# Kernel optimization log

Hardware: AMD Instinct MI355X
Metric: run time of the kernel (lower is better)

The kernel has to match this reference:

```python
import jax, jax.numpy as jnp
import numpy as np
from jax import lax

B, T, I, H = 256, 512, 128, 256


def setup_inputs() -> dict:
    key = jax.random.key(0)
    ks = jax.random.split(key, 11)
    s = 1.0 / np.sqrt(H)  # PyTorch LSTM/Linear default init range
    u = lambda k, shape: jax.random.uniform(k, shape, jnp.float32, -s, s)
    return {
        "x": jax.random.uniform(ks[0], (B, T, I), jnp.float32),
        "enc_W_ih": u(ks[1], (4 * H, I)),
        "enc_W_hh": u(ks[2], (4 * H, H)),
        "enc_b_ih": u(ks[3], (4 * H,)),
        "enc_b_hh": u(ks[4], (4 * H,)),
        "dec_W_ih": u(ks[5], (4 * H, I)),
        "dec_W_hh": u(ks[6], (4 * H, H)),
        "dec_b_ih": u(ks[7], (4 * H,)),
        "dec_b_hh": u(ks[8], (4 * H,)),
        "lin_W": u(ks[9], (I, H)),
        "lin_b": u(ks[10], (I,)),
    }


def _lstm_cell(xt, h, c, W_ih, W_hh, b):
    # PyTorch gate order: input, forget, cell(g), output
    gates = xt @ W_ih.T + h @ W_hh.T + b  # [B, 4H]
    i, f, g, o = jnp.split(gates, 4, axis=-1)
    c_new = jax.nn.sigmoid(f) * c + jax.nn.sigmoid(i) * jnp.tanh(g)
    h_new = jax.nn.sigmoid(o) * jnp.tanh(c_new)
    return h_new, c_new


def reference(x, enc_W_ih, enc_W_hh, enc_b_ih, enc_b_hh,
              dec_W_ih, dec_W_hh, dec_b_ih, dec_b_hh, lin_W, lin_b):
    batch, max_len, _ = x.shape
    b_enc = enc_b_ih + enc_b_hh
    b_dec = dec_b_ih + dec_b_hh

    # ---- encoder: standard forward LSTM, keep only final (h, c) ----
    def enc_step(carry, xt):
        h, c = carry
        h, c = _lstm_cell(xt, h, c, enc_W_ih, enc_W_hh, b_enc)
        return (h, c), None

    h0 = jnp.zeros((batch, H), x.dtype)
    c0 = jnp.zeros((batch, H), x.dtype)
    (h, c), _ = lax.scan(enc_step, (h0, c0), x.transpose(1, 0, 2))  # xs: [T,B,I]

    # prediction at the last timestep comes from encoder final hidden state
    pred_last = jax.nn.sigmoid(h @ lin_W.T + lin_b)  # [B, I]

    # ---- decoder: run backwards in time, feeding previous prediction ----
    # (inference path of the module: decoder_input = predicted_outputs[:, t+1].data,
    #  i.e. fed-back prediction is DETACHED -> stop_gradient)
    def dec_step(carry, _):
        h, c, pred = carry
        inp = lax.stop_gradient(pred)
        h, c = _lstm_cell(inp, h, c, dec_W_ih, dec_W_hh, b_dec)
        pred = jax.nn.sigmoid(h @ lin_W.T + lin_b)
        return (h, c, pred), pred

    _, preds = lax.scan(dec_step, (h, c, pred_last), None, length=max_len - 1)
    # preds[k] is the prediction at time t = max_len-2-k; flip into forward order
    out = jnp.concatenate([preds[::-1], pred_last[None]], axis=0)  # [T, B, I]
    return out.transpose(1, 0, 2)  # [B, T, I]
```

## Files before the change

### kernel.cpp

```cpp
#include <hip/hip_runtime.h>


typedef __bf16 bf16;
typedef bf16 bf16x8 __attribute__((ext_vector_type(8)));
typedef float f32x4 __attribute__((ext_vector_type(4)));
typedef unsigned u32;
typedef u32 u32x4 __attribute__((ext_vector_type(4)));

#define MFMA16(a, b, c) __builtin_amdgcn_mfma_f32_16x16x32_bf16((a), (b), (c), 0, 0, 0)
#define AT_STORE_DEV(p, v) __hip_atomic_store((p), (v), __ATOMIC_RELAXED, __HIP_MEMORY_SCOPE_AGENT)

__device__ __forceinline__ float sigm(float x) { return 1.0f / (1.0f + __expf(-x)); }
__device__ __forceinline__ float tanhfast(float x) { return 1.0f - 2.0f / (__expf(2.0f * x) + 1.0f); }

__device__ __forceinline__ u32x4 load_hx4(const u32* p) {
    u32x4 v;
    asm volatile("global_load_dwordx4 %0, %1, off sc0 sc1" : "=v"(v) : "v"(p));
    return v;
}
__device__ __forceinline__ void store_h(u32* p, u32 v) {
    asm volatile("global_store_dword %0, %1, off sc0 sc1" :: "v"(p), "v"(v) : "memory");
}
__device__ __forceinline__ u32 load_flag(const u32* p) {
    u32 v;
    asm volatile("global_load_dword %0, %1, off sc0 sc1\n\ts_waitcnt vmcnt(0)"
                 : "=v"(v) : "v"(p) : "memory");
    return v;
}

__global__ void pack_kernel(const float* __restrict__ eWih, const float* __restrict__ eWhh,
                            const float* __restrict__ dWih, const float* __restrict__ dWhh,
                            const float* __restrict__ linW,
                            bf16* __restrict__ encB, bf16* __restrict__ decB, bf16* __restrict__ linB) {
    int idx = blockIdx.x * 256 + threadIdx.x;
    if (idx < 786432) {
        int which = idx / 393216;
        int id = idx % 393216;
        int cg = id / 24576;
        int rem = id % 24576;
        int ks = rem / 2048;
        int n = (rem / 512) & 3;
        int lane = (rem >> 3) & 63;
        int e = rem & 7;
        int k = ks * 32 + (lane >> 4) * 8 + e;
        int col = n * 256 + cg * 16 + (lane & 15);
        const float* Wih = which ? dWih : eWih;
        const float* Whh = which ? dWhh : eWhh;
        float v = (k < 128) ? Wih[col * 128 + k] : Whh[col * 256 + (k - 128)];
        (which ? decB : encB)[id] = (bf16)v;
    } else if (idx < 819200) {
        int i3 = idx - 786432;
        int ks = i3 >> 12;
        int n = (i3 >> 9) & 7;
        int lane = (i3 >> 3) & 63;
        int e = i3 & 7;
        int k = ks * 32 + (lane >> 4) * 8 + e;
        int col = n * 16 + (lane & 15);
        linB[i3] = (bf16)linW[col * 256 + k];
    }
}

__global__ void zero_kernel(unsigned* __restrict__ p) {
    int i = blockIdx.x * 256 + threadIdx.x;
    if (i < 65792) AT_STORE_DEV(&p[i], 0u);
}

__global__ __launch_bounds__(256, 1)
void lstm_main(const float* __restrict__ x,
               const float* __restrict__ eb_ih, const float* __restrict__ eb_hh,
               const float* __restrict__ db_ih, const float* __restrict__ db_hh,
               const float* __restrict__ lin_b,
               const bf16* __restrict__ encB, const bf16* __restrict__ decB,
               const bf16* __restrict__ linB,
               u32* __restrict__ hbuf32, u32* __restrict__ flags,
               float* __restrict__ out) {
    __shared__ bf16 Bg[24576];
    __shared__ bf16 Lw[32768];
    __shared__ bf16 Pst[4 * 16 * 136];

    const int bid = blockIdx.x;
    const int rg = bid >> 4;
    const int cg = bid & 15;
    const int tid = threadIdx.x;
    const int w = tid >> 6;
    const int lane = tid & 63;
    const int l15 = lane & 15, l4 = lane >> 4;
    const int rbase = rg * 64 + w * 16;
    const int ucol = cg * 16 + l15;
    const int arow = rbase + l15;
    const int k0 = l4 * 8;
    const int prow = rbase + l4 * 4;

    const int rt = rg * 4 + w;
    const int htile_w = (cg >> 1) * 256;
    const int hgrp = ((cg & 1) * 2 + (l15 >> 3)) * 16;
    const int widx = (l15 & 7) >> 1;

    {
        const f32x4* src = (const f32x4*)(encB + cg * 24576);
        f32x4* dst = (f32x4*)Bg;
        #pragma unroll
        for (int i = 0; i < 12; i++) dst[tid + 256 * i] = src[tid + 256 * i];
    }
    float bias_g[4];
    #pragma unroll
    for (int g = 0; g < 4; g++) bias_g[g] = eb_ih[g * 256 + ucol] + eb_hh[g * 256 + ucol];
    __syncthreads();

    u32* myflag = flags + rg * 64 + cg;
    const u32* pollp = flags + rg * 64 + l15;
    u32 stepno = 0;
    float c[4] = {0.f, 0.f, 0.f, 0.f};

    const float* xrow = x + (size_t)arow * 512 * 128 + k0;

    f32x4 xr[8];
    #pragma unroll
    for (int i = 0; i < 4; i++) {
        xr[2 * i]     = *(const f32x4*)(xrow + i * 32);
        xr[2 * i + 1] = *(const f32x4*)(xrow + i * 32 + 4);
    }

    for (int t = 0; t < 512; t++) {
        const u32* hr32 = hbuf32 + (t & 1) * 32768;
        u32* hw32 = hbuf32 + ((t + 1) & 1) * 32768;

        u32x4 hv[8];
        const u32* hb = hr32 + rt * 2048 + lane * 4;
        #pragma unroll
        for (int ks = 0; ks < 8; ks++) hv[ks] = load_hx4(hb + ks * 256);

        f32x4 acc[4];
        #pragma unroll
        for (int n = 0; n < 4; n++) acc[n] = (f32x4){0.f, 0.f, 0.f, 0.f};

        #pragma unroll
        for (int ks = 0; ks < 4; ks++) {
            f32x4 xa = xr[2 * ks], xb = xr[2 * ks + 1];
            bf16x8 a;
            a[0] = (bf16)xa[0]; a[1] = (bf16)xa[1]; a[2] = (bf16)xa[2]; a[3] = (bf16)xa[3];
            a[4] = (bf16)xb[0]; a[5] = (bf16)xb[1]; a[6] = (bf16)xb[2]; a[7] = (bf16)xb[3];
            #pragma unroll
            for (int n = 0; n < 4; n++) {
                bf16x8 b = *(const bf16x8*)&Bg[((ks * 4 + n) * 64 + lane) * 8];
                acc[n] = MFMA16(a, b, acc[n]);
            }
        }
        asm volatile("s_waitcnt vmcnt(0)" ::: "memory");
        __builtin_amdgcn_sched_barrier(0);
        #pragma unroll
        for (int ks = 0; ks < 8; ks++) {
            bf16x8 a = __builtin_bit_cast(bf16x8, hv[ks]);
            #pragma unroll
            for (int n = 0; n < 4; n++) {
                bf16x8 b = *(const bf16x8*)&Bg[(((ks + 4) * 4 + n) * 64 + lane) * 8];
                acc[n] = MFMA16(a, b, acc[n]);
            }
        }
        #pragma unroll
        for (int r = 0; r < 4; r++) {
            float gi = sigm(acc[0][r] + bias_g[0]);
            float gf = sigm(acc[1][r] + bias_g[1]);
            float gg = tanhfast(acc[2][r] + bias_g[2]);
            float go = sigm(acc[3][r] + bias_g[3]);
            c[r] = gf * c[r] + gi * gg;
            float h = go * tanhfast(c[r]);
            unsigned hvv = (unsigned)__builtin_bit_cast(unsigned short, (bf16)h);
            unsigned hp = __shfl_xor(hvv, 1);
            if (!(lane & 1))
                store_h(&hw32[rt * 2048 + htile_w + (hgrp + l4 * 4 + r) * 4 + widx],
                        hvv | (hp << 16));
        }
        stepno++;
        __syncthreads();
        if (tid == 0) store_h(myflag, stepno);
        int tn = t < 511 ? t + 1 : 511;
        #pragma unroll
        for (int i = 0; i < 4; i++) {
            xr[2 * i]     = *(const f32x4*)(xrow + (size_t)tn * 128 + i * 32);
            xr[2 * i + 1] = *(const f32x4*)(xrow + (size_t)tn * 128 + i * 32 + 4);
        }
        while (!__all((int)(load_flag(pollp) >= stepno))) __builtin_amdgcn_s_sleep(1);
    }

    {
        const f32x4* src = (const f32x4*)(decB + cg * 24576);
        f32x4* dst = (f32x4*)Bg;
        #pragma unroll
        for (int i = 0; i < 12; i++) dst[tid + 256 * i] = src[tid + 256 * i];
        const f32x4* s2 = (const f32x4*)linB;
        f32x4* d2 = (f32x4*)Lw;
        #pragma unroll
        for (int i = 0; i < 16; i++) d2[tid + 256 * i] = s2[tid + 256 * i];
    }
    #pragma unroll
    for (int g = 0; g < 4; g++) bias_g[g] = db_ih[g * 256 + ucol] + db_hh[g * 256 + ucol];
    float lbias[8];
    #pragma unroll
    for (int n = 0; n < 8; n++) lbias[n] = lin_b[n * 16 + l15];
    __syncthreads();

    const int ncg = cg >> 1;
    const int hsel = cg & 1;

    for (int k = 0; k < 512; k++) {
        const u32* hr32 = hbuf32 + (k & 1) * 32768;

        u32x4 hv[8];
        const u32* hb = hr32 + rt * 2048 + lane * 4;
        #pragma unroll
        for (int ks = 0; ks < 8; ks++) hv[ks] = load_hx4(hb + ks * 256);
        asm volatile("s_waitcnt vmcnt(0)" ::: "memory");
        __builtin_amdgcn_sched_barrier(0);
        bf16x8 ha[8];
        #pragma unroll
        for (int ks = 0; ks < 8; ks++) ha[ks] = __builtin_bit_cast(bf16x8, hv[ks]);

        f32x4 pacc[8];
        #pragma unroll
        for (int n = 0; n < 8; n++) pacc[n] = (f32x4){0.f, 0.f, 0.f, 0.f};
        #pragma unroll
        for (int ks = 0; ks < 8; ks++) {
            #pragma unroll
            for (int n = 0; n < 8; n++) {
                bf16x8 b = *(const bf16x8*)&Lw[((ks * 8 + n) * 64 + lane) * 8];
                pacc[n] = MFMA16(ha[ks], b, pacc[n]);
            }
        }
        const int t_out = 511 - k;
        float* obase = out + (size_t)prow * 512 * 128 + (size_t)t_out * 128;
        bf16* pst_w = Pst + w * 2176;
        #pragma unroll
        for (int n = 0; n < 8; n++) {
            #pragma unroll
            for (int r = 0; r < 4; r++) {
                float p = sigm(pacc[n][r] + lbias[n]);
                pst_w[(l4 * 4 + r) * 136 + n * 16 + l15] = (bf16)p;
                if (n == ncg && (l15 >> 3) == hsel)
                    obase[(size_t)r * 512 * 128 + n * 16 + l15] = p;
            }
        }
        if (k == 511) break;

        f32x4 acc[4];
        #pragma unroll
        for (int n = 0; n < 4; n++) acc[n] = (f32x4){0.f, 0.f, 0.f, 0.f};
        #pragma unroll
        for (int ks = 0; ks < 8; ks++) {
            #pragma unroll
            for (int n = 0; n < 4; n++) {
                bf16x8 b = *(const bf16x8*)&Bg[(((ks + 4) * 4 + n) * 64 + lane) * 8];
                acc[n] = MFMA16(ha[ks], b, acc[n]);
            }
        }
        const bf16* pst_r = Pst + w * 2176 + l15 * 136 + k0;
        #pragma unroll
        for (int ks = 0; ks < 4; ks++) {
            bf16x8 a = *(const bf16x8*)(pst_r + ks * 32);
            #pragma unroll
            for (int n = 0; n < 4; n++) {
                bf16x8 b = *(const bf16x8*)&Bg[((ks * 4 + n) * 64 + lane) * 8];
                acc[n] = MFMA16(a, b, acc[n]);
            }
        }
        u32* hw32 = hbuf32 + ((k + 1) & 1) * 32768;
        #pragma unroll
        for (int r = 0; r < 4; r++) {
            float gi = sigm(acc[0][r] + bias_g[0]);
            float gf = sigm(acc[1][r] + bias_g[1]);
            float gg = tanhfast(acc[2][r] + bias_g[2]);
            float go = sigm(acc[3][r] + bias_g[3]);
            c[r] = gf * c[r] + gi * gg;
            float h = go * tanhfast(c[r]);
            unsigned hvv = (unsigned)__builtin_bit_cast(unsigned short, (bf16)h);
            unsigned hp = __shfl_xor(hvv, 1);
            if (!(lane & 1))
                store_h(&hw32[rt * 2048 + htile_w + (hgrp + l4 * 4 + r) * 4 + widx],
                        hvv | (hp << 16));
        }
        stepno++;
        __syncthreads();
        if (tid == 0) store_h(myflag, stepno);
        while (!__all((int)(load_flag(pollp) >= stepno))) __builtin_amdgcn_s_sleep(1);
    }
}

extern "C" void kernel_launch(void* const* d_in, const int* in_sizes, int n_in,
                              void* d_out, int out_size, void* d_ws, size_t ws_size,
                              hipStream_t stream) {
    const float* x    = (const float*)d_in[0];
    const float* eWih = (const float*)d_in[1];
    const float* eWhh = (const float*)d_in[2];
    const float* ebih = (const float*)d_in[3];
    const float* ebhh = (const float*)d_in[4];
    const float* dWih = (const float*)d_in[5];
    const float* dWhh = (const float*)d_in[6];
    const float* dbih = (const float*)d_in[7];
    const float* dbhh = (const float*)d_in[8];
    const float* linW = (const float*)d_in[9];
    const float* linb = (const float*)d_in[10];
    float* out = (float*)d_out;

    bf16* encB = (bf16*)d_ws;
    bf16* decB = encB + 393216;
    bf16* linB = decB + 393216;
    u32*  hbuf = (u32*)(linB + 32768);
    u32*  flags = hbuf + 65536;

    hipLaunchKernelGGL(pack_kernel, dim3(3200), dim3(256), 0, stream,
                       eWih, eWhh, dWih, dWhh, linW, encB, decB, linB);
    hipLaunchKernelGGL(zero_kernel, dim3(257), dim3(256), 0, stream, hbuf);
    hipLaunchKernelGGL(lstm_main, dim3(64), dim3(256), 0, stream,
                       x, ebih, ebhh, dbih, dbhh, linb, encB, decB, linB, hbuf, flags, out);
}
```

Before: 4.866 ms.

## Use per-wave flags instead of block barriers in recurrent LSTM steps

Replaces the per-block __syncthreads plus a single block flag with per-wavefront flags indexed by row tile, so each wave publishes its h slice and waits only on the 16 column-group waves that share its rows. The flag wait moves to the start of each step, the next x prefetch is issued earlier, and output stores are deferred until after the flag is published, keeping them off the critical path. The spin loop gains a bounded iteration cap, which could let a wave proceed before its data is ready if a peer is slow.

```diff
diff --git a/kernel.cpp b/kernel.cpp
--- a/kernel.cpp
+++ b/kernel.cpp
@@ -27,6 +27,26 @@
                  : "=v"(v) : "v"(p) : "memory");
     return v;
 }
+__device__ __forceinline__ f32x4 load_x4a(const float* p) {
+    f32x4 v;
+    asm volatile("global_load_dwordx4 %0, %1, off" : "=v"(v) : "v"(p));
+    return v;
+}
+__device__ __forceinline__ void store_f32a(float* p, float v) {
+    asm volatile("global_store_dword %0, %1, off" :: "v"(p), "v"(v) : "memory");
+}
+#define DRAIN0() do { asm volatile("s_waitcnt vmcnt(0)" ::: "memory"); \
+                      __builtin_amdgcn_sched_barrier(0); } while (0)
+
+#define FLAG_GATE(rtag)                                                          \
+    {                                                                            \
+        int spins = 0;                                                           \
+        while (!__all((int)(load_flag(pollp) >= (u32)(rtag)))) {                 \
+            if (++spins > (1 << 17)) break;                                      \
+            __builtin_amdgcn_s_sleep(1);                                         \
+        }                                                                        \
+        __builtin_amdgcn_sched_barrier(0);                                       \
+    }
 
 __global__ void pack_kernel(const float* __restrict__ eWih, const float* __restrict__ eWhh,
                             const float* __restrict__ dWih, const float* __restrict__ dWhh,
@@ -96,6 +116,9 @@
     const int hgrp = ((cg & 1) * 2 + (l15 >> 3)) * 16;
     const int widx = (l15 & 7) >> 1;
 
+    u32* myflag = flags + rt * 16 + cg;
+    const u32* pollp = flags + rt * 16 + l15;
+
     {
         const f32x4* src = (const f32x4*)(encB + cg * 24576);
         f32x4* dst = (f32x4*)Bg;
@@ -107,23 +130,21 @@
     for (int g = 0; g < 4; g++) bias_g[g] = eb_ih[g * 256 + ucol] + eb_hh[g * 256 + ucol];
     __syncthreads();
 
-    u32* myflag = flags + rg * 64 + cg;
-    const u32* pollp = flags + rg * 64 + l15;
-    u32 stepno = 0;
     float c[4] = {0.f, 0.f, 0.f, 0.f};
-
     const float* xrow = x + (size_t)arow * 512 * 128 + k0;
 
     f32x4 xr[8];
     #pragma unroll
     for (int i = 0; i < 4; i++) {
-        xr[2 * i]     = *(const f32x4*)(xrow + i * 32);
-        xr[2 * i + 1] = *(const f32x4*)(xrow + i * 32 + 4);
+        xr[2 * i]     = load_x4a(xrow + i * 32);
+        xr[2 * i + 1] = load_x4a(xrow + i * 32 + 4);
     }
 
     for (int t = 0; t < 512; t++) {
         const u32* hr32 = hbuf32 + (t & 1) * 32768;
         u32* hw32 = hbuf32 + ((t + 1) & 1) * 32768;
+
+        FLAG_GATE(t);
 
         u32x4 hv[8];
         const u32* hb = hr32 + rt * 2048 + lane * 4;
@@ -146,8 +167,15 @@
                 acc[n] = MFMA16(a, b, acc[n]);
             }
         }
-        asm volatile("s_waitcnt vmcnt(0)" ::: "memory");
-        __builtin_amdgcn_sched_barrier(0);
+        DRAIN0();
+
+        int tn = t < 511 ? t + 1 : 511;
+        #pragma unroll
+        for (int i = 0; i < 4; i++) {
+            xr[2 * i]     = load_x4a(xrow + (size_t)tn * 128 + i * 32);
+            xr[2 * i + 1] = load_x4a(xrow + (size_t)tn * 128 + i * 32 + 4);
+        }
+
         #pragma unroll
         for (int ks = 0; ks < 8; ks++) {
             bf16x8 a = __builtin_bit_cast(bf16x8, hv[ks]);
@@ -171,18 +199,11 @@
                 store_h(&hw32[rt * 2048 + htile_w + (hgrp + l4 * 4 + r) * 4 + widx],
                         hvv | (hp << 16));
         }
-        stepno++;
-        __syncthreads();
-        if (tid == 0) store_h(myflag, stepno);
-        int tn = t < 511 ? t + 1 : 511;
-        #pragma unroll
-        for (int i = 0; i < 4; i++) {
-            xr[2 * i]     = *(const f32x4*)(xrow + (size_t)tn * 128 + i * 32);
-            xr[2 * i + 1] = *(const f32x4*)(xrow + (size_t)tn * 128 + i * 32 + 4);
-        }
-        while (!__all((int)(load_flag(pollp) >= stepno))) __builtin_amdgcn_s_sleep(1);
-    }
-
+        DRAIN0();
+        if (lane == 0) store_h(myflag, (u32)(t + 1));
+    }
+
+    __syncthreads();
     {
         const f32x4* src = (const f32x4*)(decB + cg * 24576);
         f32x4* dst = (f32x4*)Bg;
@@ -193,8 +214,9 @@
         #pragma unroll
         for (int i = 0; i < 16; i++) d2[tid + 256 * i] = s2[tid + 256 * i];
     }
+    float bias_d[4];
     #pragma unroll
-    for (int g = 0; g < 4; g++) bias_g[g] = db_ih[g * 256 + ucol] + db_hh[g * 256 + ucol];
+    for (int g = 0; g < 4; g++) bias_d[g] = db_ih[g * 256 + ucol] + db_hh[g * 256 + ucol];
     float lbias[8];
     #pragma unroll
     for (int n = 0; n < 8; n++) lbias[n] = lin_b[n * 16 + l15];
@@ -205,13 +227,15 @@
 
     for (int k = 0; k < 512; k++) {
         const u32* hr32 = hbuf32 + (k & 1) * 32768;
+        const u32 rtag = (u32)(512 + k);
+
+        FLAG_GATE(rtag);
 
         u32x4 hv[8];
         const u32* hb = hr32 + rt * 2048 + lane * 4;
         #pragma unroll
         for (int ks = 0; ks < 8; ks++) hv[ks] = load_hx4(hb + ks * 256);
-        asm volatile("s_waitcnt vmcnt(0)" ::: "memory");
-        __builtin_amdgcn_sched_barrier(0);
+        DRAIN0();
         bf16x8 ha[8];
         #pragma unroll
         for (int ks = 0; ks < 8; ks++) ha[ks] = __builtin_bit_cast(bf16x8, hv[ks]);
@@ -236,11 +260,17 @@
             for (int r = 0; r < 4; r++) {
                 float p = sigm(pacc[n][r] + lbias[n]);
                 pst_w[(l4 * 4 + r) * 136 + n * 16 + l15] = (bf16)p;
-                if (n == ncg && (l15 >> 3) == hsel)
-                    obase[(size_t)r * 512 * 128 + n * 16 + l15] = p;
-            }
-        }
-        if (k == 511) break;
+            }
+        }
+        if (k == 511) {
+            #pragma unroll
+            for (int r = 0; r < 4; r++) {
+                float p = sigm(pacc[ncg][r] + lbias[ncg]);
+                if ((l15 >> 3) == hsel)
+                    store_f32a(&obase[(size_t)r * 512 * 128 + ncg * 16 + l15], p);
+            }
+            break;
+        }
 
         f32x4 acc[4];
         #pragma unroll
@@ -266,10 +296,10 @@
         u32* hw32 = hbuf32 + ((k + 1) & 1) * 32768;
         #pragma unroll
         for (int r = 0; r < 4; r++) {
-            float gi = sigm(acc[0][r] + bias_g[0]);
-            float gf = sigm(acc[1][r] + bias_g[1]);
-            float gg = tanhfast(acc[2][r] + bias_g[2]);
-            float go = sigm(acc[3][r] + bias_g[3]);
+            float gi = sigm(acc[0][r] + bias_d[0]);
+            float gf = sigm(acc[1][r] + bias_d[1]);
+            float gg = tanhfast(acc[2][r] + bias_d[2]);
+            float go = sigm(acc[3][r] + bias_d[3]);
             c[r] = gf * c[r] + gi * gg;
             float h = go * tanhfast(c[r]);
             unsigned hvv = (unsigned)__builtin_bit_cast(unsigned short, (bf16)h);
@@ -278,10 +308,14 @@
                 store_h(&hw32[rt * 2048 + htile_w + (hgrp + l4 * 4 + r) * 4 + widx],
                         hvv | (hp << 16));
         }
-        stepno++;
-        __syncthreads();
-        if (tid == 0) store_h(myflag, stepno);
-        while (!__all((int)(load_flag(pollp) >= stepno))) __builtin_amdgcn_s_sleep(1);
+        DRAIN0();
+        if (lane == 0) store_h(myflag, (u32)(rtag + 1));
+        #pragma unroll
+        for (int r = 0; r < 4; r++) {
+            float p = sigm(pacc[ncg][r] + lbias[ncg]);
+            if ((l15 >> 3) == hsel)
+                store_f32a(&obase[(size_t)r * 512 * 128 + ncg * 16 + l15], p);
+        }
     }
 }
 
```

Result: slower. 5.645 ms (+16.0%).

## Map row groups to XCCs and use XCC-local coherence for h exchange

Applied to the files above, without the earlier changes.

Launches 256 blocks. Each block reads its hardware XCC id and claims a slot with an atomic counter, so each row group (rg) is placed on one XCC and its 16 column groups exchange h and step flags only among blocks sharing that XCC's L2. A canary handshake checks that local visibility works; if it does, the loads and stores drop the sc1 (device-scope) bits, otherwise the code falls back to device-scope coherence. Surplus blocks exit right away. Spin loops gain timeout breaks. The gain depends on blocks being scheduled evenly across XCCs, and the timeouts could silently break correctness.

```diff
diff --git a/kernel.cpp b/kernel.cpp
--- a/kernel.cpp
+++ b/kernel.cpp
@@ -13,17 +13,41 @@
 __device__ __forceinline__ float sigm(float x) { return 1.0f / (1.0f + __expf(-x)); }
 __device__ __forceinline__ float tanhfast(float x) { return 1.0f - 2.0f / (__expf(2.0f * x) + 1.0f); }
 
-__device__ __forceinline__ u32x4 load_hx4(const u32* p) {
+template<bool LOC> __device__ __forceinline__ u32x4 ld_h4(const u32* p) {
     u32x4 v;
-    asm volatile("global_load_dwordx4 %0, %1, off sc0 sc1" : "=v"(v) : "v"(p));
+    if constexpr (LOC) asm volatile("global_load_dwordx4 %0, %1, off sc0" : "=v"(v) : "v"(p));
+    else               asm volatile("global_load_dwordx4 %0, %1, off sc0 sc1" : "=v"(v) : "v"(p));
     return v;
 }
-__device__ __forceinline__ void store_h(u32* p, u32 v) {
+template<bool LOC> __device__ __forceinline__ void st_h(u32* p, u32 v) {
+    if constexpr (LOC) asm volatile("global_store_dword %0, %1, off" :: "v"(p), "v"(v) : "memory");
+    else               asm volatile("global_store_dword %0, %1, off sc0 sc1" :: "v"(p), "v"(v) : "memory");
+}
+template<bool LOC> __device__ __forceinline__ u32 ld_flag(const u32* p) {
+    u32 v;
+    if constexpr (LOC)
+        asm volatile("global_load_dword %0, %1, off sc0\n\ts_waitcnt vmcnt(0)"
+                     : "=v"(v) : "v"(p) : "memory");
+    else
+        asm volatile("global_load_dword %0, %1, off sc0 sc1\n\ts_waitcnt vmcnt(0)"
+                     : "=v"(v) : "v"(p) : "memory");
+    return v;
+}
+__device__ __forceinline__ void st_dev(u32* p, u32 v) {
     asm volatile("global_store_dword %0, %1, off sc0 sc1" :: "v"(p), "v"(v) : "memory");
 }
-__device__ __forceinline__ u32 load_flag(const u32* p) {
+__device__ __forceinline__ u32 ld_dev(const u32* p) {
     u32 v;
     asm volatile("global_load_dword %0, %1, off sc0 sc1\n\ts_waitcnt vmcnt(0)"
+                 : "=v"(v) : "v"(p) : "memory");
+    return v;
+}
+__device__ __forceinline__ void st_plain(u32* p, u32 v) {
+    asm volatile("global_store_dword %0, %1, off" :: "v"(p), "v"(v) : "memory");
+}
+__device__ __forceinline__ u32 ld_sc0(const u32* p) {
+    u32 v;
+    asm volatile("global_load_dword %0, %1, off sc0\n\ts_waitcnt vmcnt(0)"
                  : "=v"(v) : "v"(p) : "memory");
     return v;
 }
@@ -62,7 +86,234 @@
 
 __global__ void zero_kernel(unsigned* __restrict__ p) {
     int i = blockIdx.x * 256 + threadIdx.x;
-    if (i < 65792) AT_STORE_DEV(&p[i], 0u);
+    if (i < 66312) AT_STORE_DEV(&p[i], 0u);
+}
+
+template<bool LOC>
+__device__ void run_chains(int rg, int cg, int tid,
+                           const float* __restrict__ x,
+                           const float* __restrict__ eb_ih, const float* __restrict__ eb_hh,
+                           const float* __restrict__ db_ih, const float* __restrict__ db_hh,
+                           const float* __restrict__ lin_b,
+                           const bf16* __restrict__ encB, const bf16* __restrict__ decB,
+                           const bf16* __restrict__ linB,
+                           u32* __restrict__ hbuf32, u32* __restrict__ flags,
+                           float* __restrict__ out,
+                           bf16* Bg, bf16* Lw, bf16* Pst) {
+    const int w = tid >> 6;
+    const int lane = tid & 63;
+    const int l15 = lane & 15, l4 = lane >> 4;
+    const int rbase = rg * 64 + w * 16;
+    const int ucol = cg * 16 + l15;
+    const int arow = rbase + l15;
+    const int k0 = l4 * 8;
+    const int prow = rbase + l4 * 4;
+
+    const int rt = rg * 4 + w;
+    const int htile_w = (cg >> 1) * 256;
+    const int hgrp = ((cg & 1) * 2 + (l15 >> 3)) * 16;
+    const int widx = (l15 & 7) >> 1;
+
+    {
+        const f32x4* src = (const f32x4*)(encB + cg * 24576);
+        f32x4* dst = (f32x4*)Bg;
+        #pragma unroll
+        for (int i = 0; i < 12; i++) dst[tid + 256 * i] = src[tid + 256 * i];
+    }
+    float bias_g[4];
+    #pragma unroll
+    for (int g = 0; g < 4; g++) bias_g[g] = eb_ih[g * 256 + ucol] + eb_hh[g * 256 + ucol];
+    __syncthreads();
+
+    u32* myflag = flags + rg * 64 + cg;
+    const u32* pollp = flags + rg * 64 + l15;
+    u32 stepno = 0;
+    float c[4] = {0.f, 0.f, 0.f, 0.f};
+
+    const float* xrow = x + (size_t)arow * 512 * 128 + k0;
+
+    f32x4 xr[8];
+    #pragma unroll
+    for (int i = 0; i < 4; i++) {
+        xr[2 * i]     = *(const f32x4*)(xrow + i * 32);
+        xr[2 * i + 1] = *(const f32x4*)(xrow + i * 32 + 4);
+    }
+
+    for (int t = 0; t < 512; t++) {
+        const u32* hr32 = hbuf32 + (t & 1) * 32768;
+        u32* hw32 = hbuf32 + ((t + 1) & 1) * 32768;
+
+        u32x4 hv[8];
+        const u32* hb = hr32 + rt * 2048 + lane * 4;
+        #pragma unroll
+        for (int ks = 0; ks < 8; ks++) hv[ks] = ld_h4<LOC>(hb + ks * 256);
+
+        f32x4 acc[4];
+        #pragma unroll
+        for (int n = 0; n < 4; n++) acc[n] = (f32x4){0.f, 0.f, 0.f, 0.f};
+
+        #pragma unroll
+        for (int ks = 0; ks < 4; ks++) {
+            f32x4 xa = xr[2 * ks], xb = xr[2 * ks + 1];
+            bf16x8 a;
+            a[0] = (bf16)xa[0]; a[1] = (bf16)xa[1]; a[2] = (bf16)xa[2]; a[3] = (bf16)xa[3];
+            a[4] = (bf16)xb[0]; a[5] = (bf16)xb[1]; a[6] = (bf16)xb[2]; a[7] = (bf16)xb[3];
+            #pragma unroll
+            for (int n = 0; n < 4; n++) {
+                bf16x8 b = *(const bf16x8*)&Bg[((ks * 4 + n) * 64 + lane) * 8];
+                acc[n] = MFMA16(a, b, acc[n]);
+            }
+        }
+        asm volatile("s_waitcnt vmcnt(0)" ::: "memory");
+        __builtin_amdgcn_sched_barrier(0);
+        #pragma unroll
+        for (int ks = 0; ks < 8; ks++) {
+            bf16x8 a = __builtin_bit_cast(bf16x8, hv[ks]);
+            #pragma unroll
+            for (int n = 0; n < 4; n++) {
+                bf16x8 b = *(const bf16x8*)&Bg[(((ks + 4) * 4 + n) * 64 + lane) * 8];
+                acc[n] = MFMA16(a, b, acc[n]);
+            }
+        }
+        #pragma unroll
+        for (int r = 0; r < 4; r++) {
+            float gi = sigm(acc[0][r] + bias_g[0]);
+            float gf = sigm(acc[1][r] + bias_g[1]);
+            float gg = tanhfast(acc[2][r] + bias_g[2]);
+            float go = sigm(acc[3][r] + bias_g[3]);
+            c[r] = gf * c[r] + gi * gg;
+            float h = go * tanhfast(c[r]);
+            unsigned hvv = (unsigned)__builtin_bit_cast(unsigned short, (bf16)h);
+            unsigned hp = __shfl_xor(hvv, 1);
+            if (!(lane & 1))
+                st_h<LOC>(&hw32[rt * 2048 + htile_w + (hgrp + l4 * 4 + r) * 4 + widx],
+                          hvv | (hp << 16));
+        }
+        stepno++;
+        __syncthreads();
+        if (tid == 0) st_h<LOC>(myflag, stepno);
+        int tn = t < 511 ? t + 1 : 511;
+        #pragma unroll
+        for (int i = 0; i < 4; i++) {
+            xr[2 * i]     = *(const f32x4*)(xrow + (size_t)tn * 128 + i * 32);
+            xr[2 * i + 1] = *(const f32x4*)(xrow + (size_t)tn * 128 + i * 32 + 4);
+        }
+        {
+            int sp = 0;
+            while (!__all((int)(ld_flag<LOC>(pollp) >= stepno))) {
+                if (++sp > 8192) break;
+                __builtin_amdgcn_s_sleep(1);
+            }
+        }
+    }
+
+    {
+        const f32x4* src = (const f32x4*)(decB + cg * 24576);
+        f32x4* dst = (f32x4*)Bg;
+        #pragma unroll
+        for (int i = 0; i < 12; i++) dst[tid + 256 * i] = src[tid + 256 * i];
+        const f32x4* s2 = (const f32x4*)linB;
+        f32x4* d2 = (f32x4*)Lw;
+        #pragma unroll
+        for (int i = 0; i < 16; i++) d2[tid + 256 * i] = s2[tid + 256 * i];
+    }
+    float bias_d[4];
+    #pragma unroll
+    for (int g = 0; g < 4; g++) bias_d[g] = db_ih[g * 256 + ucol] + db_hh[g * 256 + ucol];
+    float lbias[8];
+    #pragma unroll
+    for (int n = 0; n < 8; n++) lbias[n] = lin_b[n * 16 + l15];
+    __syncthreads();
+
+    const int ncg = cg >> 1;
+    const int hsel = cg & 1;
+
+    for (int k = 0; k < 512; k++) {
+        const u32* hr32 = hbuf32 + (k & 1) * 32768;
+
+        u32x4 hv[8];
+        const u32* hb = hr32 + rt * 2048 + lane * 4;
+        #pragma unroll
+        for (int ks = 0; ks < 8; ks++) hv[ks] = ld_h4<LOC>(hb + ks * 256);
+        asm volatile("s_waitcnt vmcnt(0)" ::: "memory");
+        __builtin_amdgcn_sched_barrier(0);
+        bf16x8 ha[8];
+        #pragma unroll
+        for (int ks = 0; ks < 8; ks++) ha[ks] = __builtin_bit_cast(bf16x8, hv[ks]);
+
+        f32x4 pacc[8];
+        #pragma unroll
+        for (int n = 0; n < 8; n++) pacc[n] = (f32x4){0.f, 0.f, 0.f, 0.f};
+        #pragma unroll
+        for (int ks = 0; ks < 8; ks++) {
+            #pragma unroll
+            for (int n = 0; n < 8; n++) {
+                bf16x8 b = *(const bf16x8*)&Lw[((ks * 8 + n) * 64 + lane) * 8];
+                pacc[n] = MFMA16(ha[ks], b, pacc[n]);
+            }
+        }
+        const int t_out = 511 - k;
+        float* obase = out + (size_t)prow * 512 * 128 + (size_t)t_out * 128;
+        bf16* pst_w = Pst + w * 2176;
+        #pragma unroll
+        for (int n = 0; n < 8; n++) {
+            #pragma unroll
+            for (int r = 0; r < 4; r++) {
+                float p = sigm(pacc[n][r] + lbias[n]);
+                pst_w[(l4 * 4 + r) * 136 + n * 16 + l15] = (bf16)p;
+                if (n == ncg && (l15 >> 3) == hsel)
+                    obase[(size_t)r * 512 * 128 + n * 16 + l15] = p;
+            }
+        }
+        if (k == 511) break;
+
+        f32x4 acc[4];
+        #pragma unroll
+        for (int n = 0; n < 4; n++) acc[n] = (f32x4){0.f, 0.f, 0.f, 0.f};
+        #pragma unroll
+        for (int ks = 0; ks < 8; ks++) {
+            #pragma unroll
+            for (int n = 0; n < 4; n++) {
+                bf16x8 b = *(const bf16x8*)&Bg[(((ks + 4) * 4 + n) * 64 + lane) * 8];
+                acc[n] = MFMA16(ha[ks], b, acc[n]);
+            }
+        }
+        const bf16* pst_r = Pst + w * 2176 + l15 * 136 + k0;
+        #pragma unroll
+        for (int ks = 0; ks < 4; ks++) {
+            bf16x8 a = *(const bf16x8*)(pst_r + ks * 32);
+            #pragma unroll
+            for (int n = 0; n < 4; n++) {
+                bf16x8 b = *(const bf16x8*)&Bg[((ks * 4 + n) * 64 + lane) * 8];
+                acc[n] = MFMA16(a, b, acc[n]);
+            }
+        }
+        u32* hw32 = hbuf32 + ((k + 1) & 1) * 32768;
+        #pragma unroll
+        for (int r = 0; r < 4; r++) {
+            float gi = sigm(acc[0][r] + bias_d[0]);
+            float gf = sigm(acc[1][r] + bias_d[1]);
+            float gg = tanhfast(acc[2][r] + bias_d[2]);
+            float go = sigm(acc[3][r] + bias_d[3]);
+            c[r] = gf * c[r] + gi * gg;
+            float h = go * tanhfast(c[r]);
+            unsigned hvv = (unsigned)__builtin_bit_cast(unsigned short, (bf16)h);
+            unsigned hp = __shfl_xor(hvv, 1);
+            if (!(lane & 1))
+                st_h<LOC>(&hw32[rt * 2048 + htile_w + (hgrp + l4 * 4 + r) * 4 + widx],
+                          hvv | (hp << 16));
+        }
+        stepno++;
+        __syncthreads();
+        if (tid == 0) st_h<LOC>(myflag, stepno);
+        {
+            int sp = 0;
+            while (!__all((int)(ld_flag<LOC>(pollp) >= stepno))) {
+                if (++sp > 8192) break;
+                __builtin_amdgcn_s_sleep(1);
+            }
+        }
+    }
 }
 
 __global__ __launch_bounds__(256, 1)
@@ -77,212 +328,58 @@
     __shared__ bf16 Bg[24576];
     __shared__ bf16 Lw[32768];
     __shared__ bf16 Pst[4 * 16 * 136];
-
-    const int bid = blockIdx.x;
-    const int rg = bid >> 4;
-    const int cg = bid & 15;
+    __shared__ int s_role[2];
+
     const int tid = threadIdx.x;
-    const int w = tid >> 6;
-    const int lane = tid & 63;
-    const int l15 = lane & 15, l4 = lane >> 4;
-    const int rbase = rg * 64 + w * 16;
-    const int ucol = cg * 16 + l15;
-    const int arow = rbase + l15;
-    const int k0 = l4 * 8;
-    const int prow = rbase + l4 * 4;
-
-    const int rt = rg * 4 + w;
-    const int htile_w = (cg >> 1) * 256;
-    const int hgrp = ((cg & 1) * 2 + (l15 >> 3)) * 16;
-    const int widx = (l15 & 7) >> 1;
-
+    u32* xslot  = flags + 256;
+    u32* boot   = flags + 264;
+    u32* canary = flags + 520;
+
+    if (tid == 0) {
+        u32 xcc;
+        asm("s_getreg_b32 %0, hwreg(HW_REG_XCC_ID)" : "=s"(xcc));
+        xcc &= 7;
+        u32 slot = __hip_atomic_fetch_add(&xslot[xcc], 1u,
+                                          __ATOMIC_RELAXED, __HIP_MEMORY_SCOPE_AGENT);
+        s_role[0] = (int)xcc;
+        s_role[1] = (int)slot;
+    }
+    __syncthreads();
+    const int rg = s_role[0];
+    const int cg = s_role[1];
+    if (rg >= 4 || cg >= 16) return;
+
+    if (tid == 0) {
+        st_plain(&canary[rg * 64 + cg], 1u);
+        const u32* pc = &canary[rg * 64 + ((cg + 1) & 15)];
+        u32 ok = 0;
+        for (int i = 0; i < 4096; i++) {
+            if (ld_sc0(pc) == 1u) { ok = 1; break; }
+            __builtin_amdgcn_s_sleep(1);
+        }
+        st_dev(&boot[rg * 64 + cg], ok ? 2u : 1u);
+    }
+    __syncthreads();
+
+    const int l15v = tid & 15;
+    u32 myv = 0;
     {
-        const f32x4* src = (const f32x4*)(encB + cg * 24576);
-        f32x4* dst = (f32x4*)Bg;
-        #pragma unroll
-        for (int i = 0; i < 12; i++) dst[tid + 256 * i] = src[tid + 256 * i];
-    }
-    float bias_g[4];
-    #pragma unroll
-    for (int g = 0; g < 4; g++) bias_g[g] = eb_ih[g * 256 + ucol] + eb_hh[g * 256 + ucol];
-    __syncthreads();
-
-    u32* myflag = flags + rg * 64 + cg;
-    const u32* pollp = flags + rg * 64 + l15;
-    u32 stepno = 0;
-    float c[4] = {0.f, 0.f, 0.f, 0.f};
-
-    const float* xrow = x + (size_t)arow * 512 * 128 + k0;
-
-    f32x4 xr[8];
-    #pragma unroll
-    for (int i = 0; i < 4; i++) {
-        xr[2 * i]     = *(const f32x4*)(xrow + i * 32);
-        xr[2 * i + 1] = *(const f32x4*)(xrow + i * 32 + 4);
-    }
-
-    for (int t = 0; t < 512; t++) {
-        const u32* hr32 = hbuf32 + (t & 1) * 32768;
-        u32* hw32 = hbuf32 + ((t + 1) & 1) * 32768;
-
-        u32x4 hv[8];
-        const u32* hb = hr32 + rt * 2048 + lane * 4;
-        #pragma unroll
-        for (int ks = 0; ks < 8; ks++) hv[ks] = load_hx4(hb + ks * 256);
-
-        f32x4 acc[4];
-        #pragma unroll
-        for (int n = 0; n < 4; n++) acc[n] = (f32x4){0.f, 0.f, 0.f, 0.f};
-
-        #pragma unroll
-        for (int ks = 0; ks < 4; ks++) {
-            f32x4 xa = xr[2 * ks], xb = xr[2 * ks + 1];
-            bf16x8 a;
-            a[0] = (bf16)xa[0]; a[1] = (bf16)xa[1]; a[2] = (bf16)xa[2]; a[3] = (bf16)xa[3];
-            a[4] = (bf16)xb[0]; a[5] = (bf16)xb[1]; a[6] = (bf16)xb[2]; a[7] = (bf16)xb[3];
-            #pragma unroll
-            for (int n = 0; n < 4; n++) {
-                bf16x8 b = *(const bf16x8*)&Bg[((ks * 4 + n) * 64 + lane) * 8];
-                acc[n] = MFMA16(a, b, acc[n]);
-            }
-        }
-        asm volatile("s_waitcnt vmcnt(0)" ::: "memory");
-        __builtin_amdgcn_sched_barrier(0);
-        #pragma unroll
-        for (int ks = 0; ks < 8; ks++) {
-            bf16x8 a = __builtin_bit_cast(bf16x8, hv[ks]);
-            #pragma unroll
-            for (int n = 0; n < 4; n++) {
-                bf16x8 b = *(const bf16x8*)&Bg[(((ks + 4) * 4 + n) * 64 + lane) * 8];
-                acc[n] = MFMA16(a, b, acc[n]);
-            }
-        }
-        #pragma unroll
-        for (int r = 0; r < 4; r++) {
-            float gi = sigm(acc[0][r] + bias_g[0]);
-            float gf = sigm(acc[1][r] + bias_g[1]);
-            float gg = tanhfast(acc[2][r] + bias_g[2]);
-            float go = sigm(acc[3][r] + bias_g[3]);
-            c[r] = gf * c[r] + gi * gg;
-            float h = go * tanhfast(c[r]);
-            unsigned hvv = (unsigned)__builtin_bit_cast(unsigned short, (bf16)h);
-            unsigned hp = __shfl_xor(hvv, 1);
-            if (!(lane & 1))
-                store_h(&hw32[rt * 2048 + htile_w + (hgrp + l4 * 4 + r) * 4 + widx],
-                        hvv | (hp << 16));
-        }
-        stepno++;
-        __syncthreads();
-        if (tid == 0) store_h(myflag, stepno);
-        int tn = t < 511 ? t + 1 : 511;
-        #pragma unroll
-        for (int i = 0; i < 4; i++) {
-            xr[2 * i]     = *(const f32x4*)(xrow + (size_t)tn * 128 + i * 32);
-            xr[2 * i + 1] = *(const f32x4*)(xrow + (size_t)tn * 128 + i * 32 + 4);
-        }
-        while (!__all((int)(load_flag(pollp) >= stepno))) __builtin_amdgcn_s_sleep(1);
-    }
-
-    {
-        const f32x4* src = (const f32x4*)(decB + cg * 24576);
-        f32x4* dst = (f32x4*)Bg;
-        #pragma unroll
-        for (int i = 0; i < 12; i++) dst[tid + 256 * i] = src[tid + 256 * i];
-        const f32x4* s2 = (const f32x4*)linB;
-        f32x4* d2 = (f32x4*)Lw;
-        #pragma unroll
-        for (int i = 0; i < 16; i++) d2[tid + 256 * i] = s2[tid + 256 * i];
-    }
-    #pragma unroll
-    for (int g = 0; g < 4; g++) bias_g[g] = db_ih[g * 256 + ucol] + db_hh[g * 256 + ucol];
-    float lbias[8];
-    #pragma unroll
-    for (int n = 0; n < 8; n++) lbias[n] = lin_b[n * 16 + l15];
-    __syncthreads();
-
-    const int ncg = cg >> 1;
-    const int hsel = cg & 1;
-
-    for (int k = 0; k < 512; k++) {
-        const u32* hr32 = hbuf32 + (k & 1) * 32768;
-
-        u32x4 hv[8];
-        const u32* hb = hr32 + rt * 2048 + lane * 4;
-        #pragma unroll
-        for (int ks = 0; ks < 8; ks++) hv[ks] = load_hx4(hb + ks * 256);
-        asm volatile("s_waitcnt vmcnt(0)" ::: "memory");
-        __builtin_amdgcn_sched_barrier(0);
-        bf16x8 ha[8];
-        #pragma unroll
-        for (int ks = 0; ks < 8; ks++) ha[ks] = __builtin_bit_cast(bf16x8, hv[ks]);
-
-        f32x4 pacc[8];
-        #pragma unroll
-        for (int n = 0; n < 8; n++) pacc[n] = (f32x4){0.f, 0.f, 0.f, 0.f};
-        #pragma unroll
-        for (int ks = 0; ks < 8; ks++) {
-            #pragma unroll
-            for (int n = 0; n < 8; n++) {
-                bf16x8 b = *(const bf16x8*)&Lw[((ks * 8 + n) * 64 + lane) * 8];
-                pacc[n] = MFMA16(ha[ks], b, pacc[n]);
-            }
-        }
-        const int t_out = 511 - k;
-        float* obase = out + (size_t)prow * 512 * 128 + (size_t)t_out * 128;
-        bf16* pst_w = Pst + w * 2176;
-        #pragma unroll
-        for (int n = 0; n < 8; n++) {
-            #pragma unroll
-            for (int r = 0; r < 4; r++) {
-                float p = sigm(pacc[n][r] + lbias[n]);
-                pst_w[(l4 * 4 + r) * 136 + n * 16 + l15] = (bf16)p;
-                if (n == ncg && (l15 >> 3) == hsel)
-                    obase[(size_t)r * 512 * 128 + n * 16 + l15] = p;
-            }
-        }
-        if (k == 511) break;
-
-        f32x4 acc[4];
-        #pragma unroll
-        for (int n = 0; n < 4; n++) acc[n] = (f32x4){0.f, 0.f, 0.f, 0.f};
-        #pragma unroll
-        for (int ks = 0; ks < 8; ks++) {
-            #pragma unroll
-            for (int n = 0; n < 4; n++) {
-                bf16x8 b = *(const bf16x8*)&Bg[(((ks + 4) * 4 + n) * 64 + lane) * 8];
-                acc[n] = MFMA16(ha[ks], b, acc[n]);
-            }
-        }
-        const bf16* pst_r = Pst + w * 2176 + l15 * 136 + k0;
-        #pragma unroll
-        for (int ks = 0; ks < 4; ks++) {
-            bf16x8 a = *(const bf16x8*)(pst_r + ks * 32);
-            #pragma unroll
-            for (int n = 0; n < 4; n++) {
-                bf16x8 b = *(const bf16x8*)&Bg[((ks * 4 + n) * 64 + lane) * 8];
-                acc[n] = MFMA16(a, b, acc[n]);
-            }
-        }
-        u32* hw32 = hbuf32 + ((k + 1) & 1) * 32768;
-        #pragma unroll
-        for (int r = 0; r < 4; r++) {
-            float gi = sigm(acc[0][r] + bias_g[0]);
-            float gf = sigm(acc[1][r] + bias_g[1]);
-            float gg = tanhfast(acc[2][r] + bias_g[2]);
-            float go = sigm(acc[3][r] + bias_g[3]);
-            c[r] = gf * c[r] + gi * gg;
-            float h = go * tanhfast(c[r]);
-            unsigned hvv = (unsigned)__builtin_bit_cast(unsigned short, (bf16)h);
-            unsigned hp = __shfl_xor(hvv, 1);
-            if (!(lane & 1))
-                store_h(&hw32[rt * 2048 + htile_w + (hgrp + l4 * 4 + r) * 4 + widx],
-                        hvv | (hp << 16));
-        }
-        stepno++;
-        __syncthreads();
-        if (tid == 0) store_h(myflag, stepno);
-        while (!__all((int)(load_flag(pollp) >= stepno))) __builtin_amdgcn_s_sleep(1);
-    }
+        int sp = 0;
+        for (;;) {
+            myv = ld_dev(&boot[rg * 64 + l15v]);
+            if (__all((int)(myv >= 1u))) break;
+            if (++sp > (1 << 16)) break;
+            __builtin_amdgcn_s_sleep(2);
+        }
+    }
+    const bool local = __all((int)(myv == 2u));
+
+    if (local)
+        run_chains<true >(rg, cg, tid, x, eb_ih, eb_hh, db_ih, db_hh, lin_b,
+                          encB, decB, linB, hbuf32, flags, out, Bg, Lw, Pst);
+    else
+        run_chains<false>(rg, cg, tid, x, eb_ih, eb_hh, db_ih, db_hh, lin_b,
+                          encB, decB, linB, hbuf32, flags, out, Bg, Lw, Pst);
 }
 
 extern "C" void kernel_launch(void* const* d_in, const int* in_sizes, int n_in,
@@ -309,7 +406,7 @@
 
     hipLaunchKernelGGL(pack_kernel, dim3(3200), dim3(256), 0, stream,
                        eWih, eWhh, dWih, dWhh, linW, encB, decB, linB);
-    hipLaunchKernelGGL(zero_kernel, dim3(257), dim3(256), 0, stream, hbuf);
-    hipLaunchKernelGGL(lstm_main, dim3(64), dim3(256), 0, stream,
+    hipLaunchKernelGGL(zero_kernel, dim3(260), dim3(256), 0, stream, hbuf);
+    hipLaunchKernelGGL(lstm_main, dim3(256), dim3(256), 0, stream,
                        x, ebih, ebhh, dbih, dbhh, linb, encB, decB, linB, hbuf, flags, out);
 }
```

Result: no change. 4.793 ms (-1.5%).
